# Optimization experiments

Hardware: AMD Instinct MI355X
Metric: run time of the kernel (lower is better)

## Reference

```python
import jax, jax.numpy as jnp
import numpy as np

B, D_IN, D_H = 32768, 512, 512


def setup_inputs() -> dict:
    key = jax.random.key(0)
    ks = jax.random.split(key, 7)
    s_in = 1.0 / np.sqrt(D_IN)
    s_h = 1.0 / np.sqrt(D_H)
    x = jax.random.normal(ks[0], (B, D_IN), dtype=jnp.float32)
    C = jax.random.normal(ks[1], (B, D_H), dtype=jnp.float32)
    h = jax.random.normal(ks[2], (B, D_H), dtype=jnp.float32)
    # Concatenated gate weights: order [i, f, o, g]. Each gate has its own
    # independent Linear(input_dim->hidden) and Linear(hidden->hidden) in torch;
    # stacking them column-wise gives identical math with 2 GEMMs.
    Wx = jax.random.uniform(ks[3], (D_IN, 4 * D_H), dtype=jnp.float32, minval=-s_in, maxval=s_in)
    bx = jax.random.uniform(ks[4], (4 * D_H,), dtype=jnp.float32, minval=-s_in, maxval=s_in)
    Wh = jax.random.uniform(ks[5], (D_H, 4 * D_H), dtype=jnp.float32, minval=-s_h, maxval=s_h)
    bh = jax.random.uniform(ks[6], (4 * D_H,), dtype=jnp.float32, minval=-s_h, maxval=s_h)
    return {"x": x, "C": C, "h": h, "Wx": Wx, "bx": bx, "Wh": Wh, "bh": bh}


def reference(x, C, h, Wx, bx, Wh, bh):
    # Two fused GEMMs replace the 8 small Linear calls (same math).
    z = x @ Wx + bx + h @ Wh + bh  # [B, 4H]
    i, f, o, g = jnp.split(z, 4, axis=-1)
    i = jax.nn.sigmoid(i)
    f = jax.nn.sigmoid(f)
    o = jax.nn.sigmoid(o)
    g = jnp.tanh(g)
    C_new = f * C + i * g
    h_new = o * jnp.tanh(C_new)
    return (C_new, h_new)
```

## Files before the change

kernel.cpp:

```cpp
#include <hip/hip_runtime.h>
#include <stdint.h>


#define BROWS 32768
#define DH 512
#define KTOT 1024
#define BM 128
#define BK 64

typedef __attribute__((ext_vector_type(8))) __bf16 bf16x8;
typedef __attribute__((ext_vector_type(4))) float f32x4;
typedef __attribute__((address_space(1))) void gvoid;
typedef __attribute__((address_space(3))) void lvoid;

__device__ __forceinline__ void gl_lds16(const void* g, void* l) {
  __builtin_amdgcn_global_load_lds((gvoid*)g, (lvoid*)l, 16, 0, 0);
}

__device__ __forceinline__ float sigf(float v)  { return 1.0f / (1.0f + __expf(-v)); }
__device__ __forceinline__ float tanhf_(float v){ return 1.0f - 2.0f / (1.0f + __expf(2.0f * v)); }

__global__ void conv_xh(const float* __restrict__ x, const float* __restrict__ h,
                        __bf16* __restrict__ xh) {
  int o = blockIdx.x * 256 + threadIdx.x;
  int c = (o & 127) * 8;
  int r = o >> 7;
  const float* src = (c < DH) ? (x + (size_t)r * DH + c)
                              : (h + (size_t)r * DH + (c - DH));
  float4 f0 = *(const float4*)src;
  float4 f1 = *(const float4*)(src + 4);
  bf16x8 v;
  v[0] = (__bf16)f0.x; v[1] = (__bf16)f0.y; v[2] = (__bf16)f0.z; v[3] = (__bf16)f0.w;
  v[4] = (__bf16)f1.x; v[5] = (__bf16)f1.y; v[6] = (__bf16)f1.z; v[7] = (__bf16)f1.w;
  *(bf16x8*)(xh + (size_t)o * 8) = v;
}

__global__ void pack_w(const float* __restrict__ Wx, const float* __restrict__ Wh,
                       __bf16* __restrict__ Wt) {
  __shared__ __bf16 T[128][72];
  const int jb = blockIdx.y;
  const int k0 = blockIdx.x * 64;
  const float* Wsrc = (k0 < DH) ? (Wx + (size_t)k0 * 4 * DH)
                                : (Wh + (size_t)(k0 - DH) * 4 * DH);
  const int t = threadIdx.x;
  const int s = t & 31, kr0 = t >> 5;
  const int g = s >> 3, q = s & 7;
  const int r0 = (q >> 2) * 64 + g * 16 + (q & 3) * 4;
  #pragma unroll
  for (int it = 0; it < 8; ++it) {
    int kr = it * 8 + kr0;
    float4 f = *(const float4*)(Wsrc + (size_t)kr * 4 * DH + g * DH + jb * 32 + q * 4);
    T[r0 + 0][kr] = (__bf16)f.x;
    T[r0 + 1][kr] = (__bf16)f.y;
    T[r0 + 2][kr] = (__bf16)f.z;
    T[r0 + 3][kr] = (__bf16)f.w;
  }
  __syncthreads();
  #pragma unroll
  for (int it = 0; it < 4; ++it) {
    int lin = it * 256 + t;
    int r = lin >> 3, k8 = lin & 7;
    bf16x8 v;
    #pragma unroll
    for (int j = 0; j < 8; ++j) v[j] = T[r][k8 * 8 + j];
    *(bf16x8*)(Wt + (size_t)(jb * 128 + r) * KTOT + k0 + k8 * 8) = v;
  }
}

#define SB __builtin_amdgcn_sched_barrier(0)
#define PH_PRE do { SB; __builtin_amdgcn_s_barrier(); \
  asm volatile("s_waitcnt lgkmcnt(0)" ::: "memory"); SB; } while (0)
#define PH_POST do { SB; __builtin_amdgcn_s_barrier(); SB; } while (0)
#define PH_POST_VM do { SB; asm volatile("s_waitcnt vmcnt(0)" ::: "memory"); \
  __builtin_amdgcn_s_barrier(); SB; } while (0)

#define STAGE_A4(PN_, kk_) do { \
  _Pragma("unroll") \
  for (int s_ = 0; s_ < 4; ++s_) { \
    const int r_ = s_ * 64 + sr; \
    gl_lds16(xh + (size_t)(row0 + r_) * KTOT + (kk_) + cs8 * 8, \
             &As[PN_][(s_ * 512 + tid) * 8]); \
  } } while (0)

#define STAGE_B2(PN_, kk_, h_) do { \
  _Pragma("unroll") \
  for (int s_ = 2 * (h_); s_ < 2 * (h_) + 2; ++s_) { \
    const int r_ = s_ * 64 + sr; \
    gl_lds16(Bt + (size_t)r_ * KTOT + (kk_) + cs8 * 8, \
             &Bs[PN_][(s_ * 512 + tid) * 8]); \
  } } while (0)

#define DS_A4(P_, cmb_, ks_) do { \
  const int cc_ = ((ks_) * 4 + q) ^ (l15 & 7); \
  _Pragma("unroll") \
  for (int i_ = 0; i_ < 4; ++i_) { \
    const int row_ = wm * 128 + ((cmb_) + i_) * 16 + l15; \
    af[i_] = *(const bf16x8*)&As[P_][row_ * 64 + cc_ * 8]; \
  } } while (0)

#define DS_B4(P_, ks_) do { \
  const int cc_ = ((ks_) * 4 + q) ^ (l15 & 7); \
  _Pragma("unroll") \
  for (int i_ = 0; i_ < 4; ++i_) { \
    const int row_ = wn * 64 + i_ * 16 + l15; \
    bfr[i_] = *(const bf16x8*)&Bs[P_][row_ * 64 + cc_ * 8]; \
  } } while (0)

#define MFMA16(cmb_) do { \
  __builtin_amdgcn_s_setprio(1); \
  _Pragma("unroll") \
  for (int i_ = 0; i_ < 4; ++i_) \
    _Pragma("unroll") \
    for (int j_ = 0; j_ < 4; ++j_) \
      acc[(cmb_) + i_][j_] = __builtin_amdgcn_mfma_f32_16x16x32_bf16( \
          af[i_], bfr[j_], acc[(cmb_) + i_][j_], 0, 0, 0); \
  __builtin_amdgcn_s_setprio(0); \
} while (0)

#define TILE(T_, P_, PN_, DOST_) do { \
  bf16x8 af[4], bfr[4]; \
   \
  DS_B4(P_, 0); DS_A4(P_, 0, 0); \
  if (DOST_) STAGE_A4(PN_, ((T_) + 1) * BK); \
  PH_PRE; MFMA16(0); PH_POST; \
   \
  DS_A4(P_, 4, 0); \
  if (DOST_) STAGE_B2(PN_, ((T_) + 1) * BK, 0); \
  PH_PRE; MFMA16(4); PH_POST; \
   \
  DS_B4(P_, 1); DS_A4(P_, 0, 1); \
  if (DOST_) STAGE_B2(PN_, ((T_) + 1) * BK, 1); \
  PH_PRE; MFMA16(0); PH_POST; \
   \
  DS_A4(P_, 4, 1); \
  PH_PRE; MFMA16(4); PH_POST_VM; \
} while (0)

__global__ __launch_bounds__(512, 2) void lstm_gemm3(
    const __bf16* __restrict__ xh, const __bf16* __restrict__ Wt,
    const float* __restrict__ bx, const float* __restrict__ bh,
    const float* __restrict__ Cin, float* __restrict__ out) {
  __shared__ __attribute__((aligned(16))) __bf16 As[2][256 * 64];
  __shared__ __attribute__((aligned(16))) __bf16 Bs[2][256 * 64];

  const int tid  = threadIdx.x;
  const int lane = tid & 63;
  const int wave = tid >> 6;
  const int wm = wave >> 2, wn = wave & 3;
  const int q = lane >> 4, l15 = lane & 15;
  const int jb   = blockIdx.x;
  const int row0 = blockIdx.y * 256;

  const __bf16* Bt = Wt + (size_t)jb * 256 * KTOT;

  const int sr  = tid >> 3;
  const int cs8 = (tid & 7) ^ (sr & 7);

  const int hd = jb * 64 + wn * 16 + l15;
  float bias[4];
  #pragma unroll
  for (int g = 0; g < 4; ++g) bias[g] = bx[g * DH + hd] + bh[g * DH + hd];

  f32x4 acc[8][4];
  #pragma unroll
  for (int a_ = 0; a_ < 8; ++a_)
    #pragma unroll
    for (int b_ = 0; b_ < 4; ++b_) acc[a_][b_] = (f32x4)0.0f;

  STAGE_A4(0, 0); STAGE_B2(0, 0, 0); STAGE_B2(0, 0, 1);
  STAGE_A4(1, BK); STAGE_B2(1, BK, 0); STAGE_B2(1, BK, 1);
  asm volatile("s_waitcnt vmcnt(8)" ::: "memory");
  __builtin_amdgcn_s_barrier();

  for (int tt = 0; tt < 16; tt += 2) {
    TILE(tt,     0, 1, (tt > 0));
    TILE(tt + 1, 1, 0, (tt < 14));
  }

  #pragma unroll
  for (int cm = 0; cm < 8; ++cm) {
    const int rbase = row0 + wm * 128 + cm * 16 + q * 4;
    #pragma unroll
    for (int i2 = 0; i2 < 4; ++i2) {
      const size_t r = (size_t)(rbase + i2);
      float cp = Cin[r * DH + hd];
      float ig = sigf(acc[cm][0][i2] + bias[0]);
      float fg = sigf(acc[cm][1][i2] + bias[1]);
      float og = sigf(acc[cm][2][i2] + bias[2]);
      float gg = tanhf_(acc[cm][3][i2] + bias[3]);
      float cnew = fg * cp + ig * gg;
      float hnew = og * tanhf_(cnew);
      __builtin_nontemporal_store(cnew, &out[r * DH + hd]);
      __builtin_nontemporal_store(hnew, &out[(size_t)BROWS * DH + r * DH + hd]);
    }
  }
}

__global__ __launch_bounds__(256, 3) void lstm_gemm(
    const float* __restrict__ x, const float* __restrict__ h,
    const __bf16* __restrict__ Wt, const float* __restrict__ bx,
    const float* __restrict__ bh, const float* __restrict__ Cin,
    float* __restrict__ out) {
  __shared__ __attribute__((aligned(16))) __bf16 Asf[BM * BK];
  __shared__ __attribute__((aligned(16))) __bf16 Bsf[BM * BK];
  const int tid  = threadIdx.x;
  const int lane = tid & 63;
  const int wave = tid >> 6;
  const int wm = wave >> 1, wn = wave & 1;
  const int jb   = blockIdx.x;
  const int row0 = blockIdx.y * BM;
  const __bf16* Bt = Wt + (size_t)jb * 128 * KTOT;
  f32x4 acc[4][4];
  #pragma unroll
  for (int a_ = 0; a_ < 4; ++a_)
    #pragma unroll
    for (int b_ = 0; b_ < 4; ++b_) acc[a_][b_] = (f32x4)0.0f;
  for (int k0 = 0; k0 < KTOT; k0 += BK) {
    const float* Aptr = (k0 < DH) ? (x + (size_t)row0 * DH + k0)
                                  : (h + (size_t)row0 * DH + (k0 - DH));
    bf16x8 ta[4], tb[4];
    #pragma unroll
    for (int it = 0; it < 4; ++it) {
      int lin = it * 256 + tid;
      int r = lin >> 3, c8 = lin & 7;
      const float* src = Aptr + r * DH + c8 * 8;
      float4 f0 = *(const float4*)src;
      float4 f1 = *(const float4*)(src + 4);
      bf16x8 v;
      v[0] = (__bf16)f0.x; v[1] = (__bf16)f0.y; v[2] = (__bf16)f0.z; v[3] = (__bf16)f0.w;
      v[4] = (__bf16)f1.x; v[5] = (__bf16)f1.y; v[6] = (__bf16)f1.z; v[7] = (__bf16)f1.w;
      ta[it] = v;
      tb[it] = *(const bf16x8*)(Bt + (size_t)r * KTOT + k0 + c8 * 8);
    }
    #pragma unroll
    for (int it = 0; it < 4; ++it) {
      int lin = it * 256 + tid;
      *(bf16x8*)&Asf[lin * 8] = ta[it];
      *(bf16x8*)&Bsf[lin * 8] = tb[it];
    }
    __syncthreads();
    #pragma unroll
    for (int ks = 0; ks < 2; ++ks) {
      const int ko = ks * 32 + (lane >> 4) * 8;
      bf16x8 af[4], bfr[4];
      #pragma unroll
      for (int cm = 0; cm < 4; ++cm)
        af[cm] = *(const bf16x8*)&Asf[(wm * 64 + cm * 16 + (lane & 15)) * BK + ko];
      #pragma unroll
      for (int cn = 0; cn < 4; ++cn)
        bfr[cn] = *(const bf16x8*)&Bsf[(wn * 64 + cn * 16 + (lane & 15)) * BK + ko];
      #pragma unroll
      for (int cm = 0; cm < 4; ++cm)
        #pragma unroll
        for (int cn = 0; cn < 4; ++cn)
          acc[cm][cn] = __builtin_amdgcn_mfma_f32_16x16x32_bf16(
              af[cm], bfr[cn], acc[cm][cn], 0, 0, 0);
    }
    __syncthreads();
  }
  const int hd = jb * 32 + wn * 16 + (lane & 15);
  float bias[4];
  #pragma unroll
  for (int g2 = 0; g2 < 4; ++g2) bias[g2] = bx[g2 * DH + hd] + bh[g2 * DH + hd];
  #pragma unroll
  for (int cm = 0; cm < 4; ++cm) {
    const int rbase = row0 + wm * 64 + cm * 16 + (lane >> 4) * 4;
    #pragma unroll
    for (int i2 = 0; i2 < 4; ++i2) {
      const size_t r = (size_t)(rbase + i2);
      float ig = sigf(acc[cm][0][i2] + bias[0]);
      float fg = sigf(acc[cm][1][i2] + bias[1]);
      float og = sigf(acc[cm][2][i2] + bias[2]);
      float gg = tanhf_(acc[cm][3][i2] + bias[3]);
      float cp = Cin[r * DH + hd];
      float cnew = fg * cp + ig * gg;
      float hnew = og * tanhf_(cnew);
      out[r * DH + hd] = cnew;
      out[(size_t)BROWS * DH + r * DH + hd] = hnew;
    }
  }
}

__global__ void lstm_naive(const float* __restrict__ x, const float* __restrict__ Cin,
                           const float* __restrict__ h, const float* __restrict__ Wx,
                           const float* __restrict__ bxp, const float* __restrict__ Wh,
                           const float* __restrict__ bhp, float* __restrict__ out) {
  int idx = blockIdx.x * 256 + threadIdx.x;
  int r = idx >> 9, hd = idx & 511;
  float z[4];
  #pragma unroll
  for (int g = 0; g < 4; ++g) z[g] = bxp[g * DH + hd] + bhp[g * DH + hd];
  for (int k = 0; k < DH; ++k) {
    float xv = x[(size_t)r * DH + k];
    #pragma unroll
    for (int g = 0; g < 4; ++g) z[g] += xv * Wx[k * 4 * DH + g * DH + hd];
  }
  for (int k = 0; k < DH; ++k) {
    float hv = h[(size_t)r * DH + k];
    #pragma unroll
    for (int g = 0; g < 4; ++g) z[g] += hv * Wh[k * 4 * DH + g * DH + hd];
  }
  float ig = sigf(z[0]), fg = sigf(z[1]), og = sigf(z[2]), gg = tanhf_(z[3]);
  float cp = Cin[(size_t)r * DH + hd];
  float cnew = fg * cp + ig * gg;
  float hnew = og * tanhf_(cnew);
  out[(size_t)r * DH + hd] = cnew;
  out[(size_t)BROWS * DH + (size_t)r * DH + hd] = hnew;
}

extern "C" void kernel_launch(void* const* d_in, const int* in_sizes, int n_in,
                              void* d_out, int out_size, void* d_ws, size_t ws_size,
                              hipStream_t stream) {
  const float* x  = (const float*)d_in[0];
  const float* Ci = (const float*)d_in[1];
  const float* h  = (const float*)d_in[2];
  const float* Wx = (const float*)d_in[3];
  const float* bx = (const float*)d_in[4];
  const float* Wh = (const float*)d_in[5];
  const float* bh = (const float*)d_in[6];
  float* out = (float*)d_out;

  const size_t wt_bytes = (size_t)2048 * KTOT * sizeof(__bf16);
  const size_t xh_bytes = (size_t)BROWS * KTOT * sizeof(__bf16);

  if (ws_size >= wt_bytes + xh_bytes) {
    __bf16* Wt = (__bf16*)d_ws;
    __bf16* xh = (__bf16*)((char*)d_ws + wt_bytes);
    pack_w<<<dim3(16, 16), dim3(256), 0, stream>>>(Wx, Wh, Wt);
    conv_xh<<<dim3((BROWS * KTOT / 8) / 256), dim3(256), 0, stream>>>(x, h, xh);
    lstm_gemm3<<<dim3(8, BROWS / 256), dim3(512), 0, stream>>>(xh, Wt, bx, bh, Ci, out);
  } else if (ws_size >= wt_bytes) {
    __bf16* Wt = (__bf16*)d_ws;
    pack_w<<<dim3(16, 16), dim3(256), 0, stream>>>(Wx, Wh, Wt);
    lstm_gemm<<<dim3(16, BROWS / BM), dim3(256), 0, stream>>>(x, h, Wt, bx, bh, Ci, out);
  } else {
    lstm_naive<<<dim3((BROWS * DH) / 256), dim3(256), 0, stream>>>(
        x, Ci, h, Wx, bx, Wh, bh, out);
  }
}
```

Before: 468.8 us.

## Switch GEMM main loop to 4-stage BK=32 LDS ring with deeper prefetch

Replaces the double-buffered BK=64 LDS pipeline with a four-buffer ring of BK=32 subtiles, prefetching three subtiles ahead and waiting with partial vmcnt counts instead of draining all loads each tile. The LDS swizzle is changed to a 4-chunk XOR pattern to match the narrower rows. The aim is to hide global-to-LDS load latency better and avoid the full vmcnt(0) stall. In exchange there are twice as many barrier-separated phases per unit of K, which adds synchronisation overhead.

New measurement: 445.7 us. 1.05x faster.

```diff
diff --git a/kernel.cpp b/kernel.cpp
--- a/kernel.cpp
+++ b/kernel.cpp
@@ -71,39 +71,41 @@
 #define PH_PRE do { SB; __builtin_amdgcn_s_barrier(); \
   asm volatile("s_waitcnt lgkmcnt(0)" ::: "memory"); SB; } while (0)
 #define PH_POST do { SB; __builtin_amdgcn_s_barrier(); SB; } while (0)
-#define PH_POST_VM do { SB; asm volatile("s_waitcnt vmcnt(0)" ::: "memory"); \
-  __builtin_amdgcn_s_barrier(); SB; } while (0)
-
-#define STAGE_A4(PN_, kk_) do { \
-  _Pragma("unroll") \
-  for (int s_ = 0; s_ < 4; ++s_) { \
-    const int r_ = s_ * 64 + sr; \
-    gl_lds16(xh + (size_t)(row0 + r_) * KTOT + (kk_) + cs8 * 8, \
-             &As[PN_][(s_ * 512 + tid) * 8]); \
+
+#define STAGE_A2(B_, kk_) do { \
+  _Pragma("unroll") \
+  for (int it_ = 0; it_ < 2; ++it_) { \
+    const int d_ = it_ * 512 + tid; \
+    const int r_ = d_ >> 2; \
+    const int c_ = (d_ & 3) ^ ((r_ >> 1) & 3); \
+    gl_lds16(xh + (size_t)(row0 + r_) * KTOT + (kk_) + c_ * 8, \
+             &As[B_][d_ * 8]); \
   } } while (0)
 
-#define STAGE_B2(PN_, kk_, h_) do { \
-  _Pragma("unroll") \
-  for (int s_ = 2 * (h_); s_ < 2 * (h_) + 2; ++s_) { \
-    const int r_ = s_ * 64 + sr; \
-    gl_lds16(Bt + (size_t)r_ * KTOT + (kk_) + cs8 * 8, \
-             &Bs[PN_][(s_ * 512 + tid) * 8]); \
+#define STAGE_B2(B_, kk_) do { \
+  _Pragma("unroll") \
+  for (int it_ = 0; it_ < 2; ++it_) { \
+    const int d_ = it_ * 512 + tid; \
+    const int r_ = d_ >> 2; \
+    const int c_ = (d_ & 3) ^ ((r_ >> 1) & 3); \
+    gl_lds16(Bt + (size_t)r_ * KTOT + (kk_) + c_ * 8, \
+             &Bs[B_][d_ * 8]); \
   } } while (0)
 
-#define DS_A4(P_, cmb_, ks_) do { \
-  const int cc_ = ((ks_) * 4 + q) ^ (l15 & 7); \
+#define DS_A4(B_, cmb_) do { \
   _Pragma("unroll") \
   for (int i_ = 0; i_ < 4; ++i_) { \
     const int row_ = wm * 128 + ((cmb_) + i_) * 16 + l15; \
-    af[i_] = *(const bf16x8*)&As[P_][row_ * 64 + cc_ * 8]; \
+    const int cp_ = q ^ ((row_ >> 1) & 3); \
+    af[i_] = *(const bf16x8*)&As[B_][row_ * 32 + cp_ * 8]; \
   } } while (0)
 
-#define DS_B4(P_, ks_) do { \
-  const int cc_ = ((ks_) * 4 + q) ^ (l15 & 7); \
+#define DS_B4(B_) do { \
   _Pragma("unroll") \
   for (int i_ = 0; i_ < 4; ++i_) { \
     const int row_ = wn * 64 + i_ * 16 + l15; \
-    bfr[i_] = *(const bf16x8*)&Bs[P_][row_ * 64 + cc_ * 8]; \
+    const int cp_ = q ^ ((row_ >> 1) & 3); \
+    bfr[i_] = *(const bf16x8*)&Bs[B_][row_ * 32 + cp_ * 8]; \
   } } while (0)
 
 #define MFMA16(cmb_) do { \
@@ -117,31 +119,32 @@
   __builtin_amdgcn_s_setprio(0); \
 } while (0)
 
-#define TILE(T_, P_, PN_, DOST_) do { \
+#define SUBTILE(S_, B_, DOST_, WC_) do { \
   bf16x8 af[4], bfr[4]; \
-   \
-  DS_B4(P_, 0); DS_A4(P_, 0, 0); \
-  if (DOST_) STAGE_A4(PN_, ((T_) + 1) * BK); \
+  DS_B4(B_); DS_A4(B_, 0); \
+  if (DOST_) STAGE_A2((B_ + 3) & 3, ((S_) + 3) * 32); \
   PH_PRE; MFMA16(0); PH_POST; \
-   \
-  DS_A4(P_, 4, 0); \
-  if (DOST_) STAGE_B2(PN_, ((T_) + 1) * BK, 0); \
-  PH_PRE; MFMA16(4); PH_POST; \
-   \
-  DS_B4(P_, 1); DS_A4(P_, 0, 1); \
-  if (DOST_) STAGE_B2(PN_, ((T_) + 1) * BK, 1); \
+  DS_A4(B_, 4); \
+  if (DOST_) STAGE_B2((B_ + 3) & 3, ((S_) + 3) * 32); \
+  PH_PRE; MFMA16(4); \
+  SB; asm volatile("s_waitcnt vmcnt(" WC_ ")" ::: "memory"); \
+  __builtin_amdgcn_s_barrier(); SB; \
+} while (0)
+
+#define SUBTILE_LAST(B_) do { \
+  bf16x8 af[4], bfr[4]; \
+  DS_B4(B_); DS_A4(B_, 0); \
   PH_PRE; MFMA16(0); PH_POST; \
-   \
-  DS_A4(P_, 4, 1); \
-  PH_PRE; MFMA16(4); PH_POST_VM; \
+  DS_A4(B_, 4); \
+  PH_PRE; MFMA16(4); \
 } while (0)
 
 __global__ __launch_bounds__(512, 2) void lstm_gemm3(
     const __bf16* __restrict__ xh, const __bf16* __restrict__ Wt,
     const float* __restrict__ bx, const float* __restrict__ bh,
     const float* __restrict__ Cin, float* __restrict__ out) {
-  __shared__ __attribute__((aligned(16))) __bf16 As[2][256 * 64];
-  __shared__ __attribute__((aligned(16))) __bf16 Bs[2][256 * 64];
+  __shared__ __attribute__((aligned(16))) __bf16 As[4][256 * 32];
+  __shared__ __attribute__((aligned(16))) __bf16 Bs[4][256 * 32];
 
   const int tid  = threadIdx.x;
   const int lane = tid & 63;
@@ -153,9 +156,6 @@
 
   const __bf16* Bt = Wt + (size_t)jb * 256 * KTOT;
 
-  const int sr  = tid >> 3;
-  const int cs8 = (tid & 7) ^ (sr & 7);
-
   const int hd = jb * 64 + wn * 16 + l15;
   float bias[4];
   #pragma unroll
@@ -167,15 +167,22 @@
     #pragma unroll
     for (int b_ = 0; b_ < 4; ++b_) acc[a_][b_] = (f32x4)0.0f;
 
-  STAGE_A4(0, 0); STAGE_B2(0, 0, 0); STAGE_B2(0, 0, 1);
-  STAGE_A4(1, BK); STAGE_B2(1, BK, 0); STAGE_B2(1, BK, 1);
-  asm volatile("s_waitcnt vmcnt(8)" ::: "memory");
-  __builtin_amdgcn_s_barrier();
-
-  for (int tt = 0; tt < 16; tt += 2) {
-    TILE(tt,     0, 1, (tt > 0));
-    TILE(tt + 1, 1, 0, (tt < 14));
-  }
+  STAGE_A2(0, 0);  STAGE_B2(0, 0);
+  STAGE_A2(1, 32); STAGE_B2(1, 32);
+  STAGE_A2(2, 64); STAGE_B2(2, 64);
+  SB; asm volatile("s_waitcnt vmcnt(8)" ::: "memory");
+  __builtin_amdgcn_s_barrier(); SB;
+
+  for (int ss = 0; ss < 28; ss += 4) {
+    SUBTILE(ss + 0, 0, 1, "8");
+    SUBTILE(ss + 1, 1, 1, "8");
+    SUBTILE(ss + 2, 2, 1, "8");
+    SUBTILE(ss + 3, 3, 1, "8");
+  }
+  SUBTILE(28, 0, 1, "8");
+  SUBTILE(29, 1, 0, "4");
+  SUBTILE(30, 2, 0, "0");
+  SUBTILE_LAST(3);
 
   #pragma unroll
   for (int cm = 0; cm < 8; ++cm) {
```
